# Performance work log

Hardware: AMD Instinct MI355X
Metric: run time of the kernel (lower is better)

## Reference

```python
import jax, jax.numpy as jnp
import numpy as np

B, L, D = 2, 2048, 1024
H = 16
HD = D // H  # 64


def setup_inputs() -> dict:
    key = jax.random.key(0)
    ks = jax.random.split(key, 7)
    s = 0.02
    return {
        "x": jax.random.normal(ks[0], (B, L, D), dtype=jnp.float32),
        "Wq": jax.random.normal(ks[1], (D, D), dtype=jnp.float32) * s,
        "bq": jnp.zeros((D,), dtype=jnp.float32),
        "Wkv": jax.random.normal(ks[2], (D, 2 * D), dtype=jnp.float32) * s,
        "bkv": jnp.zeros((2 * D,), dtype=jnp.float32),
        "Wo": jax.random.normal(ks[3], (D, D), dtype=jnp.float32) * s,
        "bo": jnp.zeros((D,), dtype=jnp.float32),
    }


def reference(x, Wq, bq, Wkv, bkv, Wo, bo):
    # q/kv projections (self-attention: key/value come from x)
    q = x @ Wq + bq                      # [B, L, D]
    kv = x @ Wkv + bkv                   # [B, L, 2D]
    k, v = jnp.split(kv, 2, axis=-1)     # each [B, L, D]
    # split heads: 'b l (h c) -> b h l c' (rope_embed_fraction=0 -> RoPE is identity)
    def heads(t):
        return t.reshape(B, L, H, HD).transpose(0, 2, 1, 3)
    qh, kh, vh = heads(q), heads(k), heads(v)   # [B, H, L, HD]
    scale = 1.0 / jnp.sqrt(jnp.asarray(HD, dtype=x.dtype))
    scores = jnp.einsum('bhqc,bhkc->bhqk', qh, kh) * scale  # [B, H, L, L]
    attn = jax.nn.softmax(scores, axis=-1)
    y = jnp.einsum('bhqk,bhkc->bhqc', attn, vh)             # [B, H, L, HD]
    # merge heads: 'b h l c -> b l (h c)'
    y = y.transpose(0, 2, 1, 3).reshape(B, L, D)
    return (y @ Wo + bo).reshape(x.shape)
```

## Files before the change

kernel.cpp:

```cpp
#include <hip/hip_runtime.h>

#define B_  2
#define L_  2048
#define D_  1024
#define H_  16
#define HD_ 64

typedef __attribute__((ext_vector_type(8))) short bf16x8;
typedef __attribute__((ext_vector_type(4))) float f32x4;

#define MFMA16(a, b, c) __builtin_amdgcn_mfma_f32_16x16x32_bf16(a, b, c, 0, 0, 0)

__device__ __forceinline__ unsigned short f2bf(float f) {
    union { float f; unsigned u; } v; v.f = f;
    unsigned r = v.u + 0x7FFFu + ((v.u >> 16) & 1u);
    return (unsigned short)(r >> 16);
}

__global__ __launch_bounds__(256) void prep_all(
    const float* __restrict__ x,
    const float* __restrict__ Wq, const float* __restrict__ Wkv,
    const float* __restrict__ Wo,
    unsigned short* __restrict__ xb,
    unsigned short* __restrict__ Wqt, unsigned short* __restrict__ Wkvt,
    unsigned short* __restrict__ Wot)
{
    const int z = blockIdx.z;
    if (z == 4) {
        const int bidl = blockIdx.y * 32 + blockIdx.x;
        const int n4 = B_ * L_ * D_ / 4;
        for (int i = bidl * 256 + threadIdx.x; i < n4; i += 1024 * 256) {
            float4 v = *(const float4*)(x + (size_t)i * 4);
            ushort4 u;
            u.x = f2bf(v.x); u.y = f2bf(v.y); u.z = f2bf(v.z); u.w = f2bf(v.w);
            *(ushort4*)(xb + (size_t)i * 4) = u;
        }
        return;
    }
    __shared__ float t[32][33];
    const float* W;  unsigned short* Wt;  int N, nc;
    if (z == 0)      { W = Wq;  Wt = Wqt;  N = 1024; nc = 0; }
    else if (z == 1) { W = Wo;  Wt = Wot;  N = 1024; nc = 0; }
    else             { W = Wkv; Wt = Wkvt; N = 2048; nc = (z - 2) * 1024; }
    const int tx = threadIdx.x & 31, ty = threadIdx.x >> 5;
    const int n0 = nc + blockIdx.x * 32, k0 = blockIdx.y * 32;
    #pragma unroll
    for (int r = 0; r < 4; ++r)
        t[ty + r * 8][tx] = W[(size_t)(k0 + ty + r * 8) * N + n0 + tx];
    __syncthreads();
    #pragma unroll
    for (int r = 0; r < 4; ++r)
        Wt[(size_t)(n0 + ty + r * 8) * 1024 + k0 + tx] = f2bf(t[tx][ty + r * 8]);
}

__global__ __launch_bounds__(512, 1) void gemm_qkv8(
    const unsigned short* __restrict__ A,
    const unsigned short* __restrict__ Bt,
    const float* __restrict__ bq, const float* __restrict__ bkv,
    unsigned short* __restrict__ Qb, unsigned short* __restrict__ Kb,
    unsigned short* __restrict__ Vtg, float qscl)
{
    const int KDIM = 1024, NT = 16;
    __shared__ __align__(16) unsigned short lds[65536];

    const int tid = threadIdx.x;
    const int w = tid >> 6, l = tid & 63, g = l >> 4, ln = l & 15;
    const int wm = (w >> 2) & 1, wn = w & 3;

    const int lin = blockIdx.x;
    const int wg = (lin & 7) * 32 + (lin >> 3);
    const int by = wg >> 3, bx = wg & 7;
    const int m0 = by * 128, n0 = bx * 384;

    const int sr8 = w * 8 + (l >> 3);
    const int sc  = (l & 7) ^ ((l >> 3) & 7);
    const unsigned short* Asrc = A  + (size_t)m0 * KDIM + sc * 8;
    const unsigned short* Bsrc = Bt + (size_t)n0 * KDIM + sc * 8;

#define SLOT_A(d, h) (lds + ((d) * 2 + (h)) * 4096)
#define SLOT_B(d, h) (lds + 16384 + ((d) * 2 + (h)) * 12288)

#define STGA(slotp, hh, kt_) do {                                             \
    const int rowA_ = (hh) * 64 + sr8;                                        \
    __builtin_amdgcn_global_load_lds(                                         \
        (const __attribute__((address_space(1))) void*)                       \
            (Asrc + (size_t)rowA_ * KDIM + (kt_) * 64),                       \
        (__attribute__((address_space(3))) void*)((slotp) + tid * 8),         \
        16, 0, 0);                                                            \
} while (0)

#define STGB(slotp, hh, kt_) do {                                             \
    _Pragma("unroll")                                                         \
    for (int r_ = 0; r_ < 3; ++r_) {                                          \
        const int rowB_ = (hh) * 192 + r_ * 64 + sr8;                         \
        __builtin_amdgcn_global_load_lds(                                     \
            (const __attribute__((address_space(1))) void*)                   \
                (Bsrc + (size_t)rowB_ * KDIM + (kt_) * 64),                   \
            (__attribute__((address_space(3))) void*)                         \
                ((slotp) + r_ * 4096 + tid * 8),                              \
            16, 0, 0);                                                        \
    }                                                                         \
} while (0)

    f32x4 acc[4][6];
    #pragma unroll
    for (int i = 0; i < 4; ++i)
        #pragma unroll
        for (int j = 0; j < 6; ++j) acc[i][j] = (f32x4){0.f, 0.f, 0.f, 0.f};

    bf16x8 aR[2][2], bB0[3][2], bB1[3][2];

    STGA(SLOT_A(0, 0), 0, 0);
    STGB(SLOT_B(0, 1), 1, 0);
    STGA(SLOT_A(0, 1), 1, 0);
    STGB(SLOT_B(0, 0), 0, 0);
    STGA(SLOT_A(1, 0), 0, 1);
    STGB(SLOT_B(1, 1), 1, 1);

    #pragma unroll 1
    for (int kt = 0; kt < NT; ++kt) {
        const int cur = kt & 1, nxt = cur ^ 1;
        const int kt1 = (kt + 1 < NT) ? kt + 1 : NT - 1;
        const int kt2 = (kt + 2 < NT) ? kt + 2 : NT - 1;
        asm volatile("s_waitcnt vmcnt(4)" ::: "memory");
        __builtin_amdgcn_s_barrier();

        #pragma unroll
        for (int mi = 0; mi < 2; ++mi)
            #pragma unroll
            for (int kc = 0; kc < 2; ++kc) {
                const int rho = wm * 32 + mi * 16 + ln, c = kc * 4 + g;
                aR[mi][kc] = *(const bf16x8*)
                    (SLOT_A(cur, 0) + rho * 64 + ((c ^ (rho & 7)) * 8));
            }
        #pragma unroll
        for (int ni = 0; ni < 3; ++ni)
            #pragma unroll
            for (int kc = 0; kc < 2; ++kc) {
                const int rho = wn * 48 + ni * 16 + ln, c = kc * 4 + g;
                bB0[ni][kc] = *(const bf16x8*)
                    (SLOT_B(cur, 0) + rho * 64 + ((c ^ (rho & 7)) * 8));
            }
        STGA(SLOT_A(nxt, 1), 1, kt1);
        __builtin_amdgcn_s_barrier();
        asm volatile("s_waitcnt lgkmcnt(0)" ::: "memory");
        __builtin_amdgcn_s_setprio(1);
        #pragma unroll
        for (int mi = 0; mi < 2; ++mi)
            #pragma unroll
            for (int ni = 0; ni < 3; ++ni) {
                acc[mi][ni] = MFMA16(aR[mi][0], bB0[ni][0], acc[mi][ni]);
                acc[mi][ni] = MFMA16(aR[mi][1], bB0[ni][1], acc[mi][ni]);
            }
        __builtin_amdgcn_s_setprio(0);
        __builtin_amdgcn_s_barrier();

        #pragma unroll
        for (int ni = 0; ni < 3; ++ni)
            #pragma unroll
            for (int kc = 0; kc < 2; ++kc) {
                const int rho = wn * 48 + ni * 16 + ln, c = kc * 4 + g;
                bB1[ni][kc] = *(const bf16x8*)
                    (SLOT_B(cur, 1) + rho * 64 + ((c ^ (rho & 7)) * 8));
            }
        STGB(SLOT_B(nxt, 0), 0, kt1);
        __builtin_amdgcn_s_barrier();
        asm volatile("s_waitcnt lgkmcnt(0)" ::: "memory");
        __builtin_amdgcn_s_setprio(1);
        #pragma unroll
        for (int mi = 0; mi < 2; ++mi)
            #pragma unroll
            for (int ni = 0; ni < 3; ++ni) {
                acc[mi][3 + ni] = MFMA16(aR[mi][0], bB1[ni][0], acc[mi][3 + ni]);
                acc[mi][3 + ni] = MFMA16(aR[mi][1], bB1[ni][1], acc[mi][3 + ni]);
            }
        __builtin_amdgcn_s_setprio(0);
        __builtin_amdgcn_s_barrier();

        #pragma unroll
        for (int mi = 0; mi < 2; ++mi)
            #pragma unroll
            for (int kc = 0; kc < 2; ++kc) {
                const int rho = wm * 32 + mi * 16 + ln, c = kc * 4 + g;
                aR[mi][kc] = *(const bf16x8*)
                    (SLOT_A(cur, 1) + rho * 64 + ((c ^ (rho & 7)) * 8));
            }
        STGA(SLOT_A(cur, 0), 0, kt2);
        __builtin_amdgcn_s_barrier();
        asm volatile("s_waitcnt lgkmcnt(0)" ::: "memory");
        __builtin_amdgcn_s_setprio(1);
        #pragma unroll
        for (int mi = 0; mi < 2; ++mi)
            #pragma unroll
            for (int ni = 0; ni < 3; ++ni) {
                acc[2 + mi][3 + ni] = MFMA16(aR[mi][0], bB1[ni][0], acc[2 + mi][3 + ni]);
                acc[2 + mi][3 + ni] = MFMA16(aR[mi][1], bB1[ni][1], acc[2 + mi][3 + ni]);
            }
        __builtin_amdgcn_s_setprio(0);
        __builtin_amdgcn_s_barrier();

        STGB(SLOT_B(cur, 1), 1, kt2);
        __builtin_amdgcn_s_barrier();
        __builtin_amdgcn_s_setprio(1);
        #pragma unroll
        for (int mi = 0; mi < 2; ++mi)
            #pragma unroll
            for (int ni = 0; ni < 3; ++ni) {
                acc[2 + mi][ni] = MFMA16(aR[mi][0], bB0[ni][0], acc[2 + mi][ni]);
                acc[2 + mi][ni] = MFMA16(aR[mi][1], bB0[ni][1], acc[2 + mi][ni]);
            }
        __builtin_amdgcn_s_setprio(0);
        __builtin_amdgcn_s_barrier();
    }
#undef STGA
#undef STGB
#undef SLOT_A
#undef SLOT_B

    #pragma unroll
    for (int nh = 0; nh < 2; ++nh)
        #pragma unroll
        for (int ni = 0; ni < 3; ++ni) {
            const int col = n0 + nh * 192 + wn * 48 + ni * 16 + ln;
            const int region = col >> 10;
            if (region == 2) {
                const int d = col - 2048;
                const float bv = bkv[1024 + d];
                #pragma unroll
                for (int mh = 0; mh < 2; ++mh)
                    #pragma unroll
                    for (int mi = 0; mi < 2; ++mi) {
                        const int tok = m0 + mh * 64 + wm * 32 + mi * 16 + g * 4;
                        const int bb = tok >> 11, t4 = tok & 2047;
                        const f32x4 av = acc[mh * 2 + mi][nh * 3 + ni];
                        ushort4 p4;
                        p4.x = f2bf(av[0] + bv); p4.y = f2bf(av[1] + bv);
                        p4.z = f2bf(av[2] + bv); p4.w = f2bf(av[3] + bv);
                        *(ushort4*)(Vtg + ((size_t)bb * 1024 + d) * 2048 + t4) = p4;
                    }
            } else {
                const int isQ = (region == 0);
                const float osc = isQ ? qscl : 1.f;
                const float bv = isQ ? bq[col] : bkv[col - 1024];
                const int ck = isQ ? col : col - 1024;
                #pragma unroll
                for (int mh = 0; mh < 2; ++mh)
                    #pragma unroll
                    for (int mi = 0; mi < 2; ++mi) {
                        const int row = m0 + mh * 64 + wm * 32 + mi * 16 + g * 4;
                        const f32x4 av = acc[mh * 2 + mi][nh * 3 + ni];
                        #pragma unroll
                        for (int r = 0; r < 4; ++r) {
                            const float vout = (av[r] + bv) * osc;
                            if (isQ)
                                Qb[(size_t)(row + r) * 1024 + ck] = f2bf(vout);
                            else
                                Kb[(size_t)(row + r) * 1024 + ck] = f2bf(vout);
                        }
                    }
            }
        }
}

__global__ __launch_bounds__(256) void gemm_bt2(
    const unsigned short* __restrict__ A,
    const unsigned short* __restrict__ Bt,
    const float* __restrict__ bias,
    float* __restrict__ Cout)
{
    const int N = 1024, K = 1024;
    __shared__ __align__(16) unsigned short As[128 * 64];
    __shared__ __align__(16) unsigned short Bs[64 * 64];
    const int tid = threadIdx.x;
    const int w = tid >> 6, l = tid & 63, g = l >> 4, ln = l & 15;
    const int wm = w >> 1, wn = w & 1;
    const int dd = blockIdx.x;
    const int bid = (dd & 7) * 64 + (dd >> 3);
    const int m0 = (bid >> 4) * 128, n0 = (bid & 15) * 64;

    const int sr8 = w * 8 + (l >> 3);
    const int sc  = (l & 7) ^ ((l >> 3) & 7);
    const unsigned short* Asrc = A  + (size_t)m0 * K + sc * 8;
    const unsigned short* Bsrc = Bt + (size_t)n0 * K + sc * 8;

    f32x4 acc[4][2];
    #pragma unroll
    for (int i = 0; i < 4; ++i)
        #pragma unroll
        for (int j = 0; j < 2; ++j) acc[i][j] = (f32x4){0.f, 0.f, 0.f, 0.f};

    for (int k0 = 0; k0 < K; k0 += 64) {
        #pragma unroll
        for (int r_ = 0; r_ < 4; ++r_)
            __builtin_amdgcn_global_load_lds(
                (const __attribute__((address_space(1))) void*)
                    (Asrc + (size_t)(r_ * 32 + sr8) * K + k0),
                (__attribute__((address_space(3))) void*)
                    (As + r_ * 2048 + w * 512 + l * 8),
                16, 0, 0);
        #pragma unroll
        for (int r_ = 0; r_ < 2; ++r_)
            __builtin_amdgcn_global_load_lds(
                (const __attribute__((address_space(1))) void*)
                    (Bsrc + (size_t)(r_ * 32 + sr8) * K + k0),
                (__attribute__((address_space(3))) void*)
                    (Bs + r_ * 2048 + w * 512 + l * 8),
                16, 0, 0);
        __syncthreads();
        bf16x8 af[4][2], bfr[2][2];
        #pragma unroll
        for (int mi = 0; mi < 4; ++mi)
            #pragma unroll
            for (int kc = 0; kc < 2; ++kc) {
                const int rho = wm * 64 + mi * 16 + ln, c = kc * 4 + g;
                af[mi][kc] = *(const bf16x8*)
                    (As + rho * 64 + ((c ^ (rho & 7)) * 8));
            }
        #pragma unroll
        for (int ni = 0; ni < 2; ++ni)
            #pragma unroll
            for (int kc = 0; kc < 2; ++kc) {
                const int rho = wn * 32 + ni * 16 + ln, c = kc * 4 + g;
                bfr[ni][kc] = *(const bf16x8*)
                    (Bs + rho * 64 + ((c ^ (rho & 7)) * 8));
            }
        __builtin_amdgcn_s_setprio(1);
        #pragma unroll
        for (int mi = 0; mi < 4; ++mi)
            #pragma unroll
            for (int ni = 0; ni < 2; ++ni) {
                acc[mi][ni] = MFMA16(af[mi][0], bfr[ni][0], acc[mi][ni]);
                acc[mi][ni] = MFMA16(af[mi][1], bfr[ni][1], acc[mi][ni]);
            }
        __builtin_amdgcn_s_setprio(0);
        __syncthreads();
    }

    #pragma unroll
    for (int n = 0; n < 2; ++n) {
        const int col = n0 + wn * 32 + n * 16 + ln;
        const float bv = bias[col];
        #pragma unroll
        for (int m = 0; m < 4; ++m) {
            const int row = m0 + wm * 64 + m * 16 + g * 4;
            #pragma unroll
            for (int r = 0; r < 4; ++r)
                Cout[(size_t)(row + r) * N + col] = acc[m][n][r] + bv;
        }
    }
}

__global__ __launch_bounds__(256, 2) void attn_mfma(
    const unsigned short* __restrict__ Qb,
    const unsigned short* __restrict__ Kb,
    const unsigned short* __restrict__ Vtg,
    unsigned short* __restrict__ Yb)
{
    __shared__ __align__(16) unsigned short Ks[2][64 * 64];
    __shared__ __align__(16) unsigned short Vs[2][64 * 64];
    __shared__ __align__(16) unsigned short Pl[4][2][32 * 64];

    const int tid = threadIdx.x;
    const int w = tid >> 6, l = tid & 63, g = l >> 4, ln = l & 15;
    const int dd = blockIdx.x;
    const int bid = (dd & 7) * 64 + (dd >> 3);
    const int qc = bid & 15, h = (bid >> 4) & 15, b = bid >> 8;
    const int qrow = b * L_ + qc * 128 + w * 32;

    const int sub = l >> 3;
    const int scc = (l & 7) ^ sub;
    const unsigned short* ksrc = Kb  + (size_t)(b * L_) * 1024 + h * HD_ + scc * 8;
    const unsigned short* vsrc = Vtg + (size_t)(b * D_ + h * HD_) * 2048 + scc * 8;

#define STAGE(jj, bb) do {                                                    \
    _Pragma("unroll")                                                         \
    for (int i_ = 0; i_ < 2; ++i_) {                                          \
        const int rowK = w * 16 + i_ * 8 + sub;                               \
        __builtin_amdgcn_global_load_lds(                                     \
            (const __attribute__((address_space(1))) void*)                   \
                (ksrc + (size_t)((jj) * 64 + rowK) * 1024),                   \
            (__attribute__((address_space(3))) void*)                         \
                (&Ks[bb][w * 1024 + i_ * 512]), 16, 0, 0);                    \
        __builtin_amdgcn_global_load_lds(                                     \
            (const __attribute__((address_space(1))) void*)                   \
                (vsrc + (size_t)rowK * 2048 + (jj) * 64),                     \
            (__attribute__((address_space(3))) void*)                         \
                (&Vs[bb][w * 1024 + i_ * 512]), 16, 0, 0);                    \
    }                                                                         \
} while (0)

    bf16x8 qa[2][2];
    #pragma unroll
    for (int qt = 0; qt < 2; ++qt)
        #pragma unroll
        for (int c = 0; c < 2; ++c)
            qa[qt][c] = *(const bf16x8*)
                (Qb + (size_t)(qrow + qt * 16 + ln) * D_ + h * HD_ + c * 32 + g * 8);

    f32x4 o[2][4], lacc[2];
    #pragma unroll
    for (int qt = 0; qt < 2; ++qt) {
        #pragma unroll
        for (int dt = 0; dt < 4; ++dt) o[qt][dt] = (f32x4){0.f, 0.f, 0.f, 0.f};
        lacc[qt] = (f32x4){0.f, 0.f, 0.f, 0.f};
    }
    const short one_s = (short)0x3F80;
    const bf16x8 ones = {one_s, one_s, one_s, one_s, one_s, one_s, one_s, one_s};

    unsigned short* Pw = &Pl[w][0][0];
    const int swzl = (ln & 7) << 3;
    const int swp  = (ln & 7) << 1;

    bf16x8 vbA[4][2], vbB[4][2];

#define S_CORE(BUF, PWS, VARR) do {                                           \
    const unsigned short* Kc = &Ks[BUF][0];                                   \
    const unsigned short* Vc = &Vs[BUF][0];                                   \
    bf16x8 kb[4][2];                                                          \
    _Pragma("unroll")                                                         \
    for (int kt = 0; kt < 4; ++kt)                                            \
        _Pragma("unroll")                                                     \
        for (int c = 0; c < 2; ++c)                                           \
            kb[kt][c] = *(const bf16x8*)                                      \
                (Kc + (kt * 16 + ln) * 64 + ((c * 32 + g * 8) ^ swzl));       \
    f32x4 s[2][4];                                                            \
    const f32x4 z = (f32x4){0.f, 0.f, 0.f, 0.f};                              \
    __builtin_amdgcn_s_setprio(1);                                            \
    _Pragma("unroll")                                                         \
    for (int qt = 0; qt < 2; ++qt)                                            \
        _Pragma("unroll")                                                     \
        for (int kt = 0; kt < 4; ++kt) {                                      \
            f32x4 t0 = MFMA16(kb[kt][0], qa[qt][0], z);                       \
            s[qt][kt] = MFMA16(kb[kt][1], qa[qt][1], t0);                     \
        }                                                                     \
    __builtin_amdgcn_s_setprio(0);                                            \
    _Pragma("unroll")                                                         \
    for (int dt = 0; dt < 4; ++dt)                                            \
        _Pragma("unroll")                                                     \
        for (int c2 = 0; c2 < 2; ++c2)                                        \
            VARR[dt][c2] = *(const bf16x8*)                                   \
                (Vc + (dt * 16 + ln) * 64 + ((c2 * 32 + g * 8) ^ swzl));      \
    _Pragma("unroll")                                                         \
    for (int qt = 0; qt < 2; ++qt) {                                          \
        const int prow = (qt * 16 + ln) * 64;                                 \
        _Pragma("unroll")                                                     \
        for (int kt = 0; kt < 4; ++kt) {                                      \
            union { float f; unsigned u; } c0, c1, c2u, c3;                   \
            c0.f = __builtin_exp2f(s[qt][kt][0]);                             \
            c1.f = __builtin_exp2f(s[qt][kt][1]);                             \
            c2u.f = __builtin_exp2f(s[qt][kt][2]);                            \
            c3.f = __builtin_exp2f(s[qt][kt][3]);                             \
            uint2 pk;                                                         \
            pk.x = __builtin_amdgcn_perm(c1.u, c0.u, 0x07060302u);            \
            pk.y = __builtin_amdgcn_perm(c3.u, c2u.u, 0x07060302u);           \
            *(uint2*)(Pw + (PWS) * 2048 + prow +                              \
                      (((kt * 4 + g) ^ swp) << 2)) = pk;                      \
        }                                                                     \
    }                                                                         \
} while (0)

#define O_PHASE(PPWS, PVARR) do {                                             \
    bf16x8 pa[2][2];                                                          \
    _Pragma("unroll")                                                         \
    for (int qt = 0; qt < 2; ++qt)                                            \
        _Pragma("unroll")                                                     \
        for (int c2 = 0; c2 < 2; ++c2)                                        \
            pa[qt][c2] = *(const bf16x8*)                                     \
                (Pw + (PPWS) * 2048 + (qt * 16 + ln) * 64 +                   \
                 (((c2 * 8 + g * 2) ^ swp) << 2));                            \
    __builtin_amdgcn_s_setprio(1);                                            \
    _Pragma("unroll")                                                         \
    for (int qt = 0; qt < 2; ++qt) {                                          \
        lacc[qt] = MFMA16(pa[qt][0], ones, lacc[qt]);                         \
        lacc[qt] = MFMA16(pa[qt][1], ones, lacc[qt]);                         \
        _Pragma("unroll")                                                     \
        for (int dt = 0; dt < 4; ++dt) {                                      \
            o[qt][dt] = MFMA16(pa[qt][0], PVARR[dt][0], o[qt][dt]);           \
            o[qt][dt] = MFMA16(pa[qt][1], PVARR[dt][1], o[qt][dt]);           \
        }                                                                     \
    }                                                                         \
    __builtin_amdgcn_s_setprio(0);                                            \
} while (0)

    STAGE(0, 0);
    __syncthreads();

    STAGE(1, 1);
    S_CORE(0, 0, vbA);
    __syncthreads();

    #pragma unroll 1
    for (int t = 1; t < 31; t += 2) {
        STAGE(t + 1, 0);
        O_PHASE(0, vbA);
        S_CORE(1, 1, vbB);
        __syncthreads();
        if (t + 2 < 32) STAGE(t + 2, 1);
        O_PHASE(1, vbB);
        S_CORE(0, 0, vbA);
        __syncthreads();
    }

    O_PHASE(0, vbA);
    S_CORE(1, 1, vbB);
    O_PHASE(1, vbB);
#undef O_PHASE
#undef S_CORE
#undef STAGE

    #pragma unroll
    for (int qt = 0; qt < 2; ++qt)
        #pragma unroll
        for (int r = 0; r < 4; ++r) {
            const float inv = 1.f / lacc[qt][r];
            const int row = qrow + qt * 16 + g * 4 + r;
            #pragma unroll
            for (int dt = 0; dt < 4; ++dt)
                Yb[(size_t)row * D_ + h * HD_ + dt * 16 + ln] =
                    f2bf(o[qt][dt][r] * inv);
        }
}

extern "C" void kernel_launch(void* const* d_in, const int* in_sizes, int n_in,
                              void* d_out, int out_size, void* d_ws, size_t ws_size,
                              hipStream_t stream)
{
    const float* x   = (const float*)d_in[0];
    const float* Wq  = (const float*)d_in[1];
    const float* bq  = (const float*)d_in[2];
    const float* Wkv = (const float*)d_in[3];
    const float* bkv = (const float*)d_in[4];
    const float* Wo  = (const float*)d_in[5];
    const float* bo  = (const float*)d_in[6];
    float* out = (float*)d_out;

    const int M = B_ * L_;
    unsigned short* ws = (unsigned short*)d_ws;
    unsigned short* xb   = ws;
    unsigned short* Wqt  = xb   + (size_t)M * D_;
    unsigned short* Wkvt = Wqt  + (size_t)D_ * D_;
    unsigned short* Wot  = Wkvt + (size_t)2 * D_ * D_;
    unsigned short* Qb   = Wot  + (size_t)D_ * D_;
    unsigned short* Kb   = Qb   + (size_t)M * D_;
    unsigned short* Vtg  = Kb   + (size_t)M * D_;
    unsigned short* Yb   = Vtg  + (size_t)B_ * D_ * L_;

    const float QSCL = 0.125f * 1.44269504089f;

    prep_all<<<dim3(32, 32, 5), 256, 0, stream>>>(
        x, Wq, Wkv, Wo, xb, Wqt, Wkvt, Wot);

    gemm_qkv8<<<dim3(256), 512, 0, stream>>>(xb, Wqt, bq, bkv, Qb, Kb, Vtg, QSCL);

    attn_mfma<<<dim3(B_ * H_ * (L_ / 128)), 256, 0, stream>>>(Qb, Kb, Vtg, Yb);

    gemm_bt2<<<dim3(512), 256, 0, stream>>>(Yb, Wot, bo, out);
}
```

Before: 119.6 us.

## Halve attention query tile per block to raise occupancy and block count

Each attention block now processes 64 query rows (16 per wave) instead of 128, doubling the grid to 1024 blocks and raising launch bounds to allow 4 blocks per CU. The per-wave P staging buffer in LDS is shrunk to a single buffer, since each wave now reads P in O_PHASE before overwriting it in S_CORE. This cuts register and LDS footprint so more waves can hide latency. In exchange, K/V tiles are loaded from global memory twice as often relative to useful work, and each wave has less independent MFMA work to overlap.

```diff
diff --git a/kernel.cpp b/kernel.cpp
--- a/kernel.cpp
+++ b/kernel.cpp
@@ -350,7 +350,7 @@
     }
 }
 
-__global__ __launch_bounds__(256, 2) void attn_mfma(
+__global__ __launch_bounds__(256, 4) void attn_mfma(
     const unsigned short* __restrict__ Qb,
     const unsigned short* __restrict__ Kb,
     const unsigned short* __restrict__ Vtg,
@@ -358,14 +358,14 @@
 {
     __shared__ __align__(16) unsigned short Ks[2][64 * 64];
     __shared__ __align__(16) unsigned short Vs[2][64 * 64];
-    __shared__ __align__(16) unsigned short Pl[4][2][32 * 64];
+    __shared__ __align__(16) unsigned short Pl[4][16 * 64];
 
     const int tid = threadIdx.x;
     const int w = tid >> 6, l = tid & 63, g = l >> 4, ln = l & 15;
     const int dd = blockIdx.x;
-    const int bid = (dd & 7) * 64 + (dd >> 3);
-    const int qc = bid & 15, h = (bid >> 4) & 15, b = bid >> 8;
-    const int qrow = b * L_ + qc * 128 + w * 32;
+    const int bid = (dd & 7) * 128 + (dd >> 3);
+    const int qc = bid & 31, h = (bid >> 5) & 15, b = bid >> 9;
+    const int qrow = b * L_ + qc * 64 + w * 16;
 
     const int sub = l >> 3;
     const int scc = (l & 7) ^ sub;
@@ -389,31 +389,26 @@
     }                                                                         \
 } while (0)
 
-    bf16x8 qa[2][2];
-    #pragma unroll
-    for (int qt = 0; qt < 2; ++qt)
-        #pragma unroll
-        for (int c = 0; c < 2; ++c)
-            qa[qt][c] = *(const bf16x8*)
-                (Qb + (size_t)(qrow + qt * 16 + ln) * D_ + h * HD_ + c * 32 + g * 8);
-
-    f32x4 o[2][4], lacc[2];
-    #pragma unroll
-    for (int qt = 0; qt < 2; ++qt) {
-        #pragma unroll
-        for (int dt = 0; dt < 4; ++dt) o[qt][dt] = (f32x4){0.f, 0.f, 0.f, 0.f};
-        lacc[qt] = (f32x4){0.f, 0.f, 0.f, 0.f};
-    }
+    bf16x8 qa[2];
+    #pragma unroll
+    for (int c = 0; c < 2; ++c)
+        qa[c] = *(const bf16x8*)
+            (Qb + (size_t)(qrow + ln) * D_ + h * HD_ + c * 32 + g * 8);
+
+    f32x4 o[4], lacc;
+    #pragma unroll
+    for (int dt = 0; dt < 4; ++dt) o[dt] = (f32x4){0.f, 0.f, 0.f, 0.f};
+    lacc = (f32x4){0.f, 0.f, 0.f, 0.f};
     const short one_s = (short)0x3F80;
     const bf16x8 ones = {one_s, one_s, one_s, one_s, one_s, one_s, one_s, one_s};
 
-    unsigned short* Pw = &Pl[w][0][0];
+    unsigned short* Pw = &Pl[w][0];
     const int swzl = (ln & 7) << 3;
     const int swp  = (ln & 7) << 1;
 
     bf16x8 vbA[4][2], vbB[4][2];
 
-#define S_CORE(BUF, PWS, VARR) do {                                           \
+#define S_CORE(BUF, VARR) do {                                                \
     const unsigned short* Kc = &Ks[BUF][0];                                   \
     const unsigned short* Vc = &Vs[BUF][0];                                   \
     bf16x8 kb[4][2];                                                          \
@@ -423,16 +418,14 @@
         for (int c = 0; c < 2; ++c)                                           \
             kb[kt][c] = *(const bf16x8*)                                      \
                 (Kc + (kt * 16 + ln) * 64 + ((c * 32 + g * 8) ^ swzl));       \
-    f32x4 s[2][4];                                                            \
+    f32x4 s[4];                                                               \
     const f32x4 z = (f32x4){0.f, 0.f, 0.f, 0.f};                              \
     __builtin_amdgcn_s_setprio(1);                                            \
     _Pragma("unroll")                                                         \
-    for (int qt = 0; qt < 2; ++qt)                                            \
-        _Pragma("unroll")                                                     \
-        for (int kt = 0; kt < 4; ++kt) {                                      \
-            f32x4 t0 = MFMA16(kb[kt][0], qa[qt][0], z);                       \
-            s[qt][kt] = MFMA16(kb[kt][1], qa[qt][1], t0);                     \
-        }                                                                     \
+    for (int kt = 0; kt < 4; ++kt) {                                          \
+        f32x4 t0 = MFMA16(kb[kt][0], qa[0], z);                               \
+        s[kt] = MFMA16(kb[kt][1], qa[1], t0);                                 \
+    }                                                                         \
     __builtin_amdgcn_s_setprio(0);                                            \
     _Pragma("unroll")                                                         \
     for (int dt = 0; dt < 4; ++dt)                                            \
@@ -440,44 +433,36 @@
         for (int c2 = 0; c2 < 2; ++c2)                                        \
             VARR[dt][c2] = *(const bf16x8*)                                   \
                 (Vc + (dt * 16 + ln) * 64 + ((c2 * 32 + g * 8) ^ swzl));      \
-    _Pragma("unroll")                                                         \
-    for (int qt = 0; qt < 2; ++qt) {                                          \
-        const int prow = (qt * 16 + ln) * 64;                                 \
+    {                                                                         \
+        const int prow = ln * 64;                                             \
         _Pragma("unroll")                                                     \
         for (int kt = 0; kt < 4; ++kt) {                                      \
             union { float f; unsigned u; } c0, c1, c2u, c3;                   \
-            c0.f = __builtin_exp2f(s[qt][kt][0]);                             \
-            c1.f = __builtin_exp2f(s[qt][kt][1]);                             \
-            c2u.f = __builtin_exp2f(s[qt][kt][2]);                            \
-            c3.f = __builtin_exp2f(s[qt][kt][3]);                             \
+            c0.f = __builtin_exp2f(s[kt][0]);                                 \
+            c1.f = __builtin_exp2f(s[kt][1]);                                 \
+            c2u.f = __builtin_exp2f(s[kt][2]);                                \
+            c3.f = __builtin_exp2f(s[kt][3]);                                 \
             uint2 pk;                                                         \
             pk.x = __builtin_amdgcn_perm(c1.u, c0.u, 0x07060302u);            \
             pk.y = __builtin_amdgcn_perm(c3.u, c2u.u, 0x07060302u);           \
-            *(uint2*)(Pw + (PWS) * 2048 + prow +                              \
-                      (((kt * 4 + g) ^ swp) << 2)) = pk;                      \
+            *(uint2*)(Pw + prow + (((kt * 4 + g) ^ swp) << 2)) = pk;          \
         }                                                                     \
     }                                                                         \
 } while (0)
 
-#define O_PHASE(PPWS, PVARR) do {                                             \
-    bf16x8 pa[2][2];                                                          \
-    _Pragma("unroll")                                                         \
-    for (int qt = 0; qt < 2; ++qt)                                            \
-        _Pragma("unroll")                                                     \
-        for (int c2 = 0; c2 < 2; ++c2)                                        \
-            pa[qt][c2] = *(const bf16x8*)                                     \
-                (Pw + (PPWS) * 2048 + (qt * 16 + ln) * 64 +                   \
-                 (((c2 * 8 + g * 2) ^ swp) << 2));                            \
+#define O_PHASE(PVARR) do {                                                   \
+    bf16x8 pa[2];                                                             \
+    _Pragma("unroll")                                                         \
+    for (int c2 = 0; c2 < 2; ++c2)                                            \
+        pa[c2] = *(const bf16x8*)                                             \
+            (Pw + ln * 64 + (((c2 * 8 + g * 2) ^ swp) << 2));                 \
     __builtin_amdgcn_s_setprio(1);                                            \
-    _Pragma("unroll")                                                         \
-    for (int qt = 0; qt < 2; ++qt) {                                          \
-        lacc[qt] = MFMA16(pa[qt][0], ones, lacc[qt]);                         \
-        lacc[qt] = MFMA16(pa[qt][1], ones, lacc[qt]);                         \
-        _Pragma("unroll")                                                     \
-        for (int dt = 0; dt < 4; ++dt) {                                      \
-            o[qt][dt] = MFMA16(pa[qt][0], PVARR[dt][0], o[qt][dt]);           \
-            o[qt][dt] = MFMA16(pa[qt][1], PVARR[dt][1], o[qt][dt]);           \
-        }                                                                     \
+    lacc = MFMA16(pa[0], ones, lacc);                                         \
+    lacc = MFMA16(pa[1], ones, lacc);                                         \
+    _Pragma("unroll")                                                         \
+    for (int dt = 0; dt < 4; ++dt) {                                          \
+        o[dt] = MFMA16(pa[0], PVARR[dt][0], o[dt]);                           \
+        o[dt] = MFMA16(pa[1], PVARR[dt][1], o[dt]);                           \
     }                                                                         \
     __builtin_amdgcn_s_setprio(0);                                            \
 } while (0)
@@ -486,39 +471,37 @@
     __syncthreads();
 
     STAGE(1, 1);
-    S_CORE(0, 0, vbA);
+    S_CORE(0, vbA);
     __syncthreads();
 
     #pragma unroll 1
     for (int t = 1; t < 31; t += 2) {
         STAGE(t + 1, 0);
-        O_PHASE(0, vbA);
-        S_CORE(1, 1, vbB);
+        O_PHASE(vbA);
+        S_CORE(1, vbB);
         __syncthreads();
         if (t + 2 < 32) STAGE(t + 2, 1);
-        O_PHASE(1, vbB);
-        S_CORE(0, 0, vbA);
+        O_PHASE(vbB);
+        S_CORE(0, vbA);
         __syncthreads();
     }
 
-    O_PHASE(0, vbA);
-    S_CORE(1, 1, vbB);
-    O_PHASE(1, vbB);
+    O_PHASE(vbA);
+    S_CORE(1, vbB);
+    O_PHASE(vbB);
 #undef O_PHASE
 #undef S_CORE
 #undef STAGE
 
     #pragma unroll
-    for (int qt = 0; qt < 2; ++qt)
-        #pragma unroll
-        for (int r = 0; r < 4; ++r) {
-            const float inv = 1.f / lacc[qt][r];
-            const int row = qrow + qt * 16 + g * 4 + r;
-            #pragma unroll
-            for (int dt = 0; dt < 4; ++dt)
-                Yb[(size_t)row * D_ + h * HD_ + dt * 16 + ln] =
-                    f2bf(o[qt][dt][r] * inv);
-        }
+    for (int r = 0; r < 4; ++r) {
+        const float inv = 1.f / lacc[r];
+        const int row = qrow + g * 4 + r;
+        #pragma unroll
+        for (int dt = 0; dt < 4; ++dt)
+            Yb[(size_t)row * D_ + h * HD_ + dt * 16 + ln] =
+                f2bf(o[dt][r] * inv);
+    }
 }
 
 extern "C" void kernel_launch(void* const* d_in, const int* in_sizes, int n_in,
@@ -552,7 +535,7 @@
 
     gemm_qkv8<<<dim3(256), 512, 0, stream>>>(xb, Wqt, bq, bkv, Qb, Kb, Vtg, QSCL);
 
-    attn_mfma<<<dim3(B_ * H_ * (L_ / 128)), 256, 0, stream>>>(Qb, Kb, Vtg, Yb);
+    attn_mfma<<<dim3(1024), 256, 0, stream>>>(Qb, Kb, Vtg, Yb);
 
     gemm_bt2<<<dim3(512), 256, 0, stream>>>(Yb, Wot, bo, out);
 }
```

Result: no change. 121.1 us (median of 2 runs) (+1.2%).
